# Performance work log

Hardware: AMD Instinct MI355X
Metric: run time of the kernel (lower is better)

## Reference

```python
import jax, jax.numpy as jnp
import numpy as np

N_NODES = 50000
N_EDGES = 800000
F_IN = 128


def setup_inputs() -> dict:
    key = jax.random.key(0)
    ks = jax.random.split(key, 8)
    x = jax.random.normal(ks[0], (N_NODES, F_IN), dtype=jnp.float32)
    edge_index = jax.random.randint(ks[1], (2, N_EDGES), 0, N_NODES, dtype=jnp.int64)
    def lin(k, fan_in, fan_out):
        bound = 1.0 / np.sqrt(fan_in)
        return jax.random.uniform(k, (fan_in, fan_out), jnp.float32, -bound, bound)
    W1 = lin(ks[2], F_IN, 64)
    W2 = lin(ks[3], 64, 64)
    W3 = lin(ks[4], 64, 64)
    Wf1 = lin(ks[5], 64, 32)
    Wf2 = lin(ks[6], 32, 1)
    return {
        'x': x, 'edge_index': edge_index,
        'W1': W1, 'b1': jnp.zeros((64,), jnp.float32),
        'W2': W2, 'b2': jnp.zeros((64,), jnp.float32),
        'W3': W3, 'b3': jnp.zeros((64,), jnp.float32),
        'Wf1': Wf1, 'bf1': jnp.zeros((32,), jnp.float32),
        'Wf2': Wf2, 'bf2': jnp.zeros((1,), jnp.float32),
    }


def reference(x, edge_index, W1, b1, W2, b2, W3, b3, Wf1, bf1, Wf2, bf2):
    row, col = edge_index[0], edge_index[1]
    for W, b in ((W1, b1), (W2, b2), (W3, b3)):
        agg = jax.ops.segment_sum(x[col], row, num_segments=N_NODES)  # [N, d]
        x = jax.nn.relu(agg @ W + b)
    h = x.mean(axis=0)                      # [64] global mean pool
    h = jax.nn.relu(h @ Wf1 + bf1)          # [32]
    out = jax.nn.sigmoid(h @ Wf2 + bf2)     # [1]
    return out
```

## Files before the change

kernel.cpp:

```cpp
#include <hip/hip_runtime.h>
#include <hip/hip_bf16.h>
#include <math.h>

#define N_NODES 50000
#define N_EDGES 800000
#define CAP 64
#define PAD_ROW 65535

typedef float v2f __attribute__((ext_vector_type(2)));

__device__ __forceinline__ unsigned int pack4_fp8(float f0, float f1,
                                                  float f2, float f3) {
    unsigned int p = 0;
    p = __builtin_amdgcn_cvt_pk_fp8_f32(f0, f1, p, false);
    p = __builtin_amdgcn_cvt_pk_fp8_f32(f2, f3, p, true);
    return p;
}

__device__ __forceinline__ float fp8_lo(unsigned int b) {
    const v2f t = __builtin_amdgcn_cvt_pk_f32_fp8(b, false);
    return t.x;
}

template <int K>
__global__ __launch_bounds__(256) void gemm_plain(
    const float* __restrict__ in, const float* __restrict__ W,
    unsigned int* __restrict__ out8, int N)
{
    __shared__ float Wl[K * 64];
    __shared__ float xs[32][K];

    const int tid = threadIdx.x;
    const int j   = tid & 63;
    const int rq  = tid >> 6;
    const int base = blockIdx.x * 32;

    for (int i = tid; i < K * 64; i += 256) Wl[i] = W[i];

    for (int i = tid; i < 32 * K; i += 256) {
        const int r = i / K;
        const int k = i - r * K;
        float v = 0.f;
        if (base + r < N) v = in[(size_t)(base + r) * K + k];
        xs[r][k] = v;
    }
    __syncthreads();

    float acc[8];
#pragma unroll
    for (int rr = 0; rr < 8; ++rr) acc[rr] = 0.f;

    for (int k = 0; k < K; ++k) {
        const float wv = Wl[k * 64 + j];
#pragma unroll
        for (int rr = 0; rr < 8; ++rr)
            acc[rr] += xs[rq + rr * 4][k] * wv;
    }

    __syncthreads();
#pragma unroll
    for (int rr = 0; rr < 8; ++rr) xs[rq + rr * 4][j] = acc[rr];
    __syncthreads();
#pragma unroll
    for (int m = 0; m < 2; ++m) {
        const int idx = m * 256 + tid;
        const int r2 = idx >> 4;
        const int c4 = idx & 15;
        const int row = base + r2;
        if (row < N) {
            const unsigned int p = pack4_fp8(
                xs[r2][c4 * 4 + 0], xs[r2][c4 * 4 + 1],
                xs[r2][c4 * 4 + 2], xs[r2][c4 * 4 + 3]);
            out8[(size_t)row * 16 + c4] = p;
        }
    }
}

__global__ __launch_bounds__(256) void gemm_act64(
    const float* __restrict__ agg, const float* __restrict__ W,
    const float* __restrict__ bias, unsigned int* __restrict__ out8, int N)
{
    __shared__ float Wl[64 * 64];
    __shared__ float xs[32][64];

    const int tid = threadIdx.x;
    const int j   = tid & 63;
    const int rq  = tid >> 6;
    const int base = blockIdx.x * 32;

    for (int i = tid; i < 64 * 64; i += 256) Wl[i] = W[i];

    for (int i = tid; i < 32 * 64; i += 256) {
        const int r = i >> 6;
        const int k = i & 63;
        float v = 0.f;
        if (base + r < N) v = fmaxf(agg[(size_t)(base + r) * 64 + k] + bias[k], 0.f);
        xs[r][k] = v;
    }
    __syncthreads();

    float acc[8];
#pragma unroll
    for (int rr = 0; rr < 8; ++rr) acc[rr] = 0.f;

    for (int k = 0; k < 64; ++k) {
        const float wv = Wl[k * 64 + j];
#pragma unroll
        for (int rr = 0; rr < 8; ++rr)
            acc[rr] += xs[rq + rr * 4][k] * wv;
    }

    __syncthreads();
#pragma unroll
    for (int rr = 0; rr < 8; ++rr) xs[rq + rr * 4][j] = acc[rr];
    __syncthreads();
#pragma unroll
    for (int m = 0; m < 2; ++m) {
        const int idx = m * 256 + tid;
        const int r2 = idx >> 4;
        const int c4 = idx & 15;
        const int row = base + r2;
        if (row < N) {
            const unsigned int p = pack4_fp8(
                xs[r2][c4 * 4 + 0], xs[r2][c4 * 4 + 1],
                xs[r2][c4 * 4 + 2], xs[r2][c4 * 4 + 3]);
            out8[(size_t)row * 16 + c4] = p;
        }
    }
}

__global__ __launch_bounds__(256) void build_bucket(
    const int* __restrict__ rowv, const int* __restrict__ colv,
    int* __restrict__ cnt, unsigned short* __restrict__ buck, int E)
{
    const int e = blockIdx.x * 256 + threadIdx.x;
    if (e >= E) return;
    const int r = rowv[e];
    const int slot = atomicAdd(&cnt[r], 1);
    if (slot < CAP) buck[r * CAP + slot] = (unsigned short)colv[e];
}

__device__ __forceinline__ float gather16(
    const unsigned char* __restrict__ y8b, int bval, int lane, const int base)
{
    float s0 = 0.f, s1 = 0.f, s2 = 0.f, s3 = 0.f;
#pragma unroll
    for (int k = 0; k < 16; k += 4) {
        const int c0 = __builtin_amdgcn_readlane(bval, base + k + 0);
        const int c1 = __builtin_amdgcn_readlane(bval, base + k + 1);
        const int c2 = __builtin_amdgcn_readlane(bval, base + k + 2);
        const int c3 = __builtin_amdgcn_readlane(bval, base + k + 3);
        const unsigned int b0 = y8b[(size_t)c0 * 64 + lane];
        const unsigned int b1 = y8b[(size_t)c1 * 64 + lane];
        const unsigned int b2 = y8b[(size_t)c2 * 64 + lane];
        const unsigned int b3 = y8b[(size_t)c3 * 64 + lane];
        s0 += fp8_lo(b0);
        s1 += fp8_lo(b1);
        s2 += fp8_lo(b2);
        s3 += fp8_lo(b3);
    }
    return (s0 + s1) + (s2 + s3);
}

__device__ __forceinline__ float node_accum(
    const unsigned char* __restrict__ y8b, const int* __restrict__ cnt,
    const unsigned short* __restrict__ buck, int n, int lane)
{
    int c0 = cnt[n]; if (c0 > CAP) c0 = CAP;
    const int bval = (int)buck[n * CAP + lane];
    float acc = 0.f;
    if (c0 > 0)  acc += gather16(y8b, bval, lane, 0);
    if (c0 > 16) acc += gather16(y8b, bval, lane, 16);
    if (c0 > 32) acc += gather16(y8b, bval, lane, 32);
    if (c0 > 48) acc += gather16(y8b, bval, lane, 48);
    return acc;
}

__global__ __launch_bounds__(256) void aggregate_b(
    const unsigned char* __restrict__ y8b, const int* __restrict__ cnt,
    const unsigned short* __restrict__ buck, float* __restrict__ agg, int N)
{
    const int w    = threadIdx.x >> 6;
    const int lane = threadIdx.x & 63;
    const int n = blockIdx.x * 4 + w;
    if (n >= N) return;
    const float acc = node_accum(y8b, cnt, buck, n, lane);
    agg[(size_t)n * 64 + lane] = acc;
}

__global__ __launch_bounds__(256) void agg_pool(
    const unsigned char* __restrict__ y8b, const int* __restrict__ cnt,
    const unsigned short* __restrict__ buck, const float* __restrict__ bias,
    float* __restrict__ hpart, int N)
{
    const int tid  = threadIdx.x;
    const int w    = tid >> 6;
    const int lane = tid & 63;
    const float b  = bias[lane];

    float s = 0.f;
    for (int n = blockIdx.x * 4 + w; n < N; n += gridDim.x * 4) {
        const float acc = node_accum(y8b, cnt, buck, n, lane);
        s += fmaxf(acc + b, 0.f);
    }

    __shared__ float red[4][64];
    red[w][lane] = s;
    __syncthreads();
    if (tid < 64) {
        const float t = red[0][tid] + red[1][tid] + red[2][tid] + red[3][tid];
        atomicAdd(&hpart[tid], t);
    }
}

__global__ __launch_bounds__(64) void head_kernel(
    const float* __restrict__ hpart, const float* __restrict__ Wf1,
    const float* __restrict__ bf1, const float* __restrict__ Wf2,
    const float* __restrict__ bf2, float* __restrict__ out, float invN)
{
    __shared__ float hm[64];
    __shared__ float t[32];
    const int tid = threadIdx.x;
    hm[tid] = hpart[tid] * invN;
    __syncthreads();
    if (tid < 32) {
        float a = bf1[tid];
        for (int k = 0; k < 64; ++k) a += hm[k] * Wf1[k * 32 + tid];
        t[tid] = fmaxf(a, 0.f);
    }
    __syncthreads();
    if (tid == 0) {
        float a = bf2[0];
        for (int i = 0; i < 32; ++i) a += t[i] * Wf2[i];
        out[0] = 1.f / (1.f + expf(-a));
    }
}

extern "C" void kernel_launch(void* const* d_in, const int* in_sizes, int n_in,
                              void* d_out, int out_size, void* d_ws, size_t ws_size,
                              hipStream_t stream)
{
    const float* x   = (const float*)d_in[0];
    const int*   ei  = (const int*)d_in[1];
    const float* W1  = (const float*)d_in[2];
    const float* b1  = (const float*)d_in[3];
    const float* W2  = (const float*)d_in[4];
    const float* b2  = (const float*)d_in[5];
    const float* W3  = (const float*)d_in[6];
    const float* b3  = (const float*)d_in[7];
    const float* Wf1 = (const float*)d_in[8];
    const float* bf1 = (const float*)d_in[9];
    const float* Wf2 = (const float*)d_in[10];
    const float* bf2 = (const float*)d_in[11];
    float* out = (float*)d_out;

    const int N = N_NODES;
    const int E = N_EDGES;
    const int* rowv = ei;
    const int* colv = ei + E;

    float*          aggf  = (float*)d_ws;
    unsigned char*  y8b   = (unsigned char*)(aggf + (size_t)N * 64);
    float*          hpart = (float*)(y8b + (size_t)65536 * 64);
    int*            cnt   = (int*)(hpart + 64);
    unsigned short* buck  = (unsigned short*)(cnt + N);

    const int gemmGrid = (N + 31) / 32;
    const int edgeGrid = (E + 255) / 256;
    const int aggGrid  = (N + 3) / 4;

    hipMemsetAsync(cnt, 0, (size_t)N * sizeof(int), stream);
    hipMemsetAsync(buck, 0xFF, (size_t)N * CAP * sizeof(unsigned short), stream);
    hipMemsetAsync(y8b + (size_t)PAD_ROW * 64, 0, 64, stream);
    build_bucket<<<edgeGrid, 256, 0, stream>>>(rowv, colv, cnt, buck, E);

    gemm_plain<128><<<gemmGrid, 256, 0, stream>>>(x, W1, (unsigned int*)y8b, N);
    aggregate_b<<<aggGrid, 256, 0, stream>>>(y8b, cnt, buck, aggf, N);

    gemm_act64<<<gemmGrid, 256, 0, stream>>>(aggf, W2, b1, (unsigned int*)y8b, N);
    aggregate_b<<<aggGrid, 256, 0, stream>>>(y8b, cnt, buck, aggf, N);

    gemm_act64<<<gemmGrid, 256, 0, stream>>>(aggf, W3, b2, (unsigned int*)y8b, N);
    hipMemsetAsync(hpart, 0, 64 * sizeof(float), stream);
    agg_pool<<<1024, 256, 0, stream>>>(y8b, cnt, buck, b3, hpart, N);
    head_kernel<<<1, 64, 0, stream>>>(hpart, Wf1, bf1, Wf2, bf2, out,
                                      1.0f / (float)N);
}
```

Baseline: 291.2 us.

## Fuse edge bucketing into first GEMM launch and vectorize GEMM inner loops

Merges the build_bucket kernel into the first GEMM kernel. Blocks are interleaved so one in three does the 128-wide GEMM and the other two each bucket 256 edges, letting the two independent stages overlap and saving one launch. The GEMM inner loops also read four k values at a time from shared memory as float4 to cut LDS instructions. The fused kernel's bucketing blocks still declare the large shared-memory arrays, which may reduce how many blocks fit per CU.

```diff
diff --git a/kernel.cpp b/kernel.cpp
--- a/kernel.cpp
+++ b/kernel.cpp
@@ -22,26 +22,44 @@
     return t.x;
 }
 
-template <int K>
-__global__ __launch_bounds__(256) void gemm_plain(
+__global__ __launch_bounds__(256) void gemm_build(
     const float* __restrict__ in, const float* __restrict__ W,
-    unsigned int* __restrict__ out8, int N)
-{
-    __shared__ float Wl[K * 64];
-    __shared__ float xs[32][K];
-
+    unsigned int* __restrict__ out8, int N,
+    const int* __restrict__ rowv, const int* __restrict__ colv,
+    int* __restrict__ cnt, unsigned short* __restrict__ buck, int E,
+    int gemmGrid)
+{
+    __shared__ float Wl[128 * 64];
+    __shared__ float xs[32][128];
+
+    const int bid = blockIdx.x;
+    const int grp = bid / 3;
+    const int rem = bid - grp * 3;
     const int tid = threadIdx.x;
-    const int j   = tid & 63;
-    const int rq  = tid >> 6;
-    const int base = blockIdx.x * 32;
-
-    for (int i = tid; i < K * 64; i += 256) Wl[i] = W[i];
-
-    for (int i = tid; i < 32 * K; i += 256) {
-        const int r = i / K;
-        const int k = i - r * K;
+
+    if (rem != 0) {
+        const int widx = grp * 2 + (rem - 1);
+        const int e = widx * 256 + tid;
+        if (e < E) {
+            const int r = rowv[e];
+            const int slot = atomicAdd(&cnt[r], 1);
+            if (slot < CAP) buck[r * CAP + slot] = (unsigned short)colv[e];
+        }
+        return;
+    }
+
+    if (grp >= gemmGrid) return;
+    const int j    = tid & 63;
+    const int rq   = tid >> 6;
+    const int base = grp * 32;
+
+    for (int i = tid; i < 128 * 64; i += 256) Wl[i] = W[i];
+
+    for (int i = tid; i < 32 * 128; i += 256) {
+        const int r = i >> 7;
+        const int k = i & 127;
         float v = 0.f;
-        if (base + r < N) v = in[(size_t)(base + r) * K + k];
+        if (base + r < N) v = in[(size_t)(base + r) * 128 + k];
         xs[r][k] = v;
     }
     __syncthreads();
@@ -50,11 +68,16 @@
 #pragma unroll
     for (int rr = 0; rr < 8; ++rr) acc[rr] = 0.f;
 
-    for (int k = 0; k < K; ++k) {
-        const float wv = Wl[k * 64 + j];
-#pragma unroll
-        for (int rr = 0; rr < 8; ++rr)
-            acc[rr] += xs[rq + rr * 4][k] * wv;
+    for (int k = 0; k < 128; k += 4) {
+        const float wv0 = Wl[(k + 0) * 64 + j];
+        const float wv1 = Wl[(k + 1) * 64 + j];
+        const float wv2 = Wl[(k + 2) * 64 + j];
+        const float wv3 = Wl[(k + 3) * 64 + j];
+#pragma unroll
+        for (int rr = 0; rr < 8; ++rr) {
+            const float4 xv = *(const float4*)&xs[rq + rr * 4][k];
+            acc[rr] += xv.x * wv0 + xv.y * wv1 + xv.z * wv2 + xv.w * wv3;
+        }
     }
 
     __syncthreads();
@@ -103,11 +126,16 @@
 #pragma unroll
     for (int rr = 0; rr < 8; ++rr) acc[rr] = 0.f;
 
-    for (int k = 0; k < 64; ++k) {
-        const float wv = Wl[k * 64 + j];
-#pragma unroll
-        for (int rr = 0; rr < 8; ++rr)
-            acc[rr] += xs[rq + rr * 4][k] * wv;
+    for (int k = 0; k < 64; k += 4) {
+        const float wv0 = Wl[(k + 0) * 64 + j];
+        const float wv1 = Wl[(k + 1) * 64 + j];
+        const float wv2 = Wl[(k + 2) * 64 + j];
+        const float wv3 = Wl[(k + 3) * 64 + j];
+#pragma unroll
+        for (int rr = 0; rr < 8; ++rr) {
+            const float4 xv = *(const float4*)&xs[rq + rr * 4][k];
+            acc[rr] += xv.x * wv0 + xv.y * wv1 + xv.z * wv2 + xv.w * wv3;
+        }
     }
 
     __syncthreads();
@@ -127,17 +155,6 @@
             out8[(size_t)row * 16 + c4] = p;
         }
     }
-}
-
-__global__ __launch_bounds__(256) void build_bucket(
-    const int* __restrict__ rowv, const int* __restrict__ colv,
-    int* __restrict__ cnt, unsigned short* __restrict__ buck, int E)
-{
-    const int e = blockIdx.x * 256 + threadIdx.x;
-    if (e >= E) return;
-    const int r = rowv[e];
-    const int slot = atomicAdd(&cnt[r], 1);
-    if (slot < CAP) buck[r * CAP + slot] = (unsigned short)colv[e];
 }
 
 __device__ __forceinline__ float gather16(
@@ -266,15 +283,15 @@
     unsigned short* buck  = (unsigned short*)(cnt + N);
 
     const int gemmGrid = (N + 31) / 32;
-    const int edgeGrid = (E + 255) / 256;
     const int aggGrid  = (N + 3) / 4;
 
     hipMemsetAsync(cnt, 0, (size_t)N * sizeof(int), stream);
     hipMemsetAsync(buck, 0xFF, (size_t)N * CAP * sizeof(unsigned short), stream);
     hipMemsetAsync(y8b + (size_t)PAD_ROW * 64, 0, 64, stream);
-    build_bucket<<<edgeGrid, 256, 0, stream>>>(rowv, colv, cnt, buck, E);
-
-    gemm_plain<128><<<gemmGrid, 256, 0, stream>>>(x, W1, (unsigned int*)y8b, N);
+
+    gemm_build<<<gemmGrid * 3, 256, 0, stream>>>(
+        x, W1, (unsigned int*)y8b, N, rowv, colv, cnt, buck, E, gemmGrid);
+
     aggregate_b<<<aggGrid, 256, 0, stream>>>(y8b, cnt, buck, aggf, N);
 
     gemm_act64<<<gemmGrid, 256, 0, stream>>>(aggf, W2, b1, (unsigned int*)y8b, N);
```

Result: faster. 261.7 us (-10.2%).
